# Kernel optimization log

Hardware: AMD Instinct MI355X
Metric: run time of the kernel (lower is better)

The kernel has to match this reference:

```python
import jax, jax.numpy as jnp
import numpy as np

TEMP = 0.07
EPS = 1e-8
THRESH = 0.0          # self.global_threshold default
NORM_EPS = 1e-12      # F.normalize default eps


def setup_inputs() -> dict:
    key = jax.random.key(0)
    k1, k2, k3 = jax.random.split(key, 3)
    T, C, H, W = 8, 256, 64, 64
    return {
        "current_preds": jax.random.uniform(k1, (T, 1, H, W), jnp.float32),
        "history_preds": jax.random.uniform(k2, (T, 1, H, W), jnp.float32),
        "features": jax.random.normal(k3, (T, C, H, W), jnp.float32),
        "epoch": 1,
    }


def _supervised_labels(current_preds, history_preds):
    # Deviation per video (Dice-like metrics on binarized preds), then select
    # current pred if dev <= threshold else history pred (both detached).
    T = current_preds.shape[0]
    cb = (current_preds > 0.5).astype(jnp.float32).reshape(T, -1)
    hb = (history_preds > 0.5).astype(jnp.float32).reshape(T, -1)
    e1 = (cb * hb).sum(axis=1)
    e2 = cb.sum(axis=1) + hb.sum(axis=1)
    m1 = (2.0 * e1 + EPS) / (e2 + EPS)
    m2 = (e1 + EPS) / (e2 - e1 + EPS)
    dev = 1.0 - (m1 + m2) / 2.0                       # [T]
    use_curr = (dev <= THRESH)[:, None, None, None]
    return jnp.where(use_curr, current_preds, history_preds)


def _contrastive_loss(features, labels):
    T, C, H, W = features.shape
    N = H * W
    feat = features.reshape(T, C, N).transpose(0, 2, 1)            # [T,N,C]
    nrm = jnp.linalg.norm(feat, axis=-1, keepdims=True)
    feat = feat / jnp.maximum(nrm, NORM_EPS)                       # L2 normalize
    lbl = labels.reshape(T, N)
    fg = lbl > 0.5
    bg = ~fg
    sim = jnp.einsum('tnc,tmc->tnm', feat, feat) / TEMP            # [T,N,N]
    pos = jnp.exp(jnp.diagonal(sim, axis1=1, axis2=2))             # [T,N]
    # neg_i = sum over bg columns of exp(sim); masked matvec honors fg/bg split
    neg = jnp.einsum('tnm,tm->tn', jnp.exp(sim), bg.astype(feat.dtype))
    per_pix = -jnp.log(pos / (pos + neg + EPS))                    # [T,N]
    fgf = fg.astype(feat.dtype)
    n_fg = fgf.sum(axis=1)
    frame_loss = (per_pix * fgf).sum(axis=1) / jnp.maximum(n_fg, 1.0)  # mean over fg
    valid = (fg.any(axis=1) & bg.any(axis=1)).astype(feat.dtype)   # frames with both
    n_valid = valid.sum()
    return jnp.where(n_valid > 0,
                     (frame_loss * valid).sum() / jnp.maximum(n_valid, 1.0),
                     jnp.zeros((), feat.dtype))


def reference(current_preds, history_preds, features, epoch):
    # epoch >= 1 path of DOC.forward (epoch==0 only populates memory)
    labels = jax.lax.stop_gradient(_supervised_labels(current_preds, history_preds))
    loss = _contrastive_loss(features, labels)
    return (labels, loss)
```

## Files before the change

kernel.cpp:

```cpp
#include <hip/hip_runtime.h>
#include <hip/hip_bf16.h>
#include <cstdint>
#include <cstddef>

constexpr int T = 8;
constexpr int C = 256;
constexpr int N = 4096;
constexpr int CAP = 4232;
constexpr float TEMP_INV = 14.285714285714286f;
constexpr float EPS = 1e-8f;

typedef __bf16 bf16;
typedef __bf16 bf16x8 __attribute__((ext_vector_type(8)));
typedef float floatx4 __attribute__((ext_vector_type(4)));

__device__ __forceinline__ void async_copy16(const bf16* g, bf16* l) {
    __builtin_amdgcn_global_load_lds((const __attribute__((address_space(1))) void*)g,
                                     (__attribute__((address_space(3))) void*)l,
                                     16, 0, 0);
}

__global__ void prep_kernel(const float* __restrict__ cur,
                            const float* __restrict__ hist,
                            float* __restrict__ out_labels,
                            float* __restrict__ negbuf,
                            unsigned short* __restrict__ rankmap,
                            bf16* __restrict__ fpack,
                            int* __restrict__ nfg, int* __restrict__ nbg) {
    int t = blockIdx.x;
    int tid = threadIdx.x;
    int lane = tid & 63;
    int w = tid >> 6;

    float cv[4], hv[4];
    float s1 = 0.f, sc = 0.f, sh = 0.f;
    #pragma unroll
    for (int it = 0; it < 4; ++it) {
        int p = it * 1024 + tid;
        float c = cur[t * N + p];
        float h = hist[t * N + p];
        cv[it] = c; hv[it] = h;
        float cb = c > 0.5f ? 1.f : 0.f;
        float hb = h > 0.5f ? 1.f : 0.f;
        s1 += cb * hb; sc += cb; sh += hb;
    }
    for (int o = 32; o > 0; o >>= 1) {
        s1 += __shfl_down(s1, o);
        sc += __shfl_down(sc, o);
        sh += __shfl_down(sh, o);
    }
    __shared__ float r1[16], r2[16], r3[16];
    __shared__ float uflag;
    __shared__ int cfg_s, cbg_s;
    if (lane == 0) { r1[w] = s1; r2[w] = sc; r3[w] = sh; }
    if (tid == 0) { cfg_s = 0; cbg_s = 0; }
    __syncthreads();
    if (tid == 0) {
        float e1 = 0.f, scs = 0.f, shs = 0.f;
        for (int i = 0; i < 16; ++i) { e1 += r1[i]; scs += r2[i]; shs += r3[i]; }
        float e2 = scs + shs;
        float m1 = (2.f * e1 + EPS) / (e2 + EPS);
        float m2 = (e1 + EPS) / (e2 - e1 + EPS);
        float dev = 1.f - 0.5f * (m1 + m2);
        uflag = (dev <= 0.0f) ? 1.f : 0.f;
    }
    __syncthreads();
    bool use_curr = uflag != 0.f;
    for (int it = 0; it < 4; ++it) {
        int p = it * 1024 + tid;
        int gi = t * N + p;
        float lab = use_curr ? cv[it] : hv[it];
        out_labels[gi] = lab;
        negbuf[gi] = 0.f;
        bool fg = lab > 0.5f;
        unsigned long long b = __ballot(fg);
        unsigned long long lowmask = (lane == 63) ? 0x7fffffffffffffffull
                                                  : ((1ull << lane) - 1ull);
        int rank_fg = __popcll(b & lowmask);
        int rank_bg = __popcll((~b) & lowmask);
        int cnt_fg = __popcll(b);
        int base_fg = 0, base_bg = 0;
        if (lane == 0) {
            base_fg = atomicAdd(&cfg_s, cnt_fg);
            base_bg = atomicAdd(&cbg_s, 64 - cnt_fg);
        }
        base_fg = __shfl(base_fg, 0);
        base_bg = __shfl(base_bg, 0);
        int rank = fg ? (base_fg + rank_fg) : (base_bg + rank_bg);
        rankmap[gi] = (unsigned short)(rank | (fg ? 0x8000 : 0));
    }
    __syncthreads();
    if (tid == 0) { nfg[t] = cfg_s; nbg[t] = cbg_s; }
    float4 z4 = make_float4(0.f, 0.f, 0.f, 0.f);
    float4* pz = (float4*)(fpack + ((size_t)t * CAP + N) * C);
    int chunks = (CAP - N) * (C / 8);
    for (int i = tid; i < chunks; i += 1024) pz[i] = z4;
}

__global__ __launch_bounds__(256, 4) void normalize_kernel(const float* __restrict__ feat,
                                                           const unsigned short* __restrict__ rankmap,
                                                           const int* __restrict__ nfg,
                                                           bf16* __restrict__ fpack,
                                                           float* __restrict__ posc) {
    __shared__ bf16 tile[64 * 258];
    __shared__ float partial[256];
    __shared__ float rnorm_s[64];
    __shared__ unsigned short rk_s[64];
    __shared__ int bbase_s;
    int t = blockIdx.x & 7;
    int n0 = (blockIdx.x >> 3) * 64;
    int tid = threadIdx.x;
    int lane63 = tid & 63;
    int w = tid >> 6;
    if (tid == 0) bbase_s = (nfg[t] + 7) & ~7;
    if (tid < 64) rk_s[tid] = rankmap[t * N + n0 + tid];
    const float* fb = feat + (size_t)t * C * N;
    float ss = 0.f;
    #pragma unroll 16
    for (int it = 0; it < 64; ++it) {
        int c = w * 64 + it;
        float v = fb[(size_t)c * N + n0 + lane63];
        ss += v * v;
        tile[lane63 * 258 + c] = (bf16)v;
    }
    partial[tid] = ss;
    __syncthreads();
    if (tid < 64) {
        float s = partial[tid] + partial[tid + 64] + partial[tid + 128] + partial[tid + 192];
        float r = 1.f / fmaxf(sqrtf(s), 1e-12f);
        rnorm_s[tid] = r;
        unsigned short rk = rk_s[tid];
        if (rk & 0x8000) posc[t * N + (rk & 0x7fff)] = s * r * r;
    }
    __syncthreads();
    int bbase = bbase_s;
    bf16* fp = fpack + (size_t)t * CAP * C;
    #pragma unroll
    for (int it = 0; it < 8; ++it) {
        int l = it * 256 + tid;
        int n = l >> 5;
        int c8 = l & 31;
        unsigned short rk = rk_s[n];
        int r_pack = (rk & 0x7fff) + ((rk & 0x8000) ? 0 : bbase);
        int slot = (c8 & ~7) | ((c8 & 7) ^ (r_pack & 7));
        float r = rnorm_s[n];
        bf16x8 vin = *(const bf16x8*)&tile[n * 258 + c8 * 8];
        bf16x8 vo;
        for (int j = 0; j < 8; ++j) vo[j] = (bf16)((float)vin[j] * r);
        *(bf16x8*)(fp + (size_t)r_pack * C + slot * 8) = vo;
    }
}

__global__ __launch_bounds__(256, 3) void sim_kernel(const bf16* __restrict__ fpack,
                                                     const int* __restrict__ nfg,
                                                     const int* __restrict__ nbg,
                                                     float* __restrict__ neg) {
    int t = blockIdx.x & 7;
    int wid = blockIdx.x >> 3;
    int nfgt = nfg[t];
    int nbgt = nbg[t];
    if (nfgt <= 0 || nbgt <= 0) return;
    int nr = (nfgt + 127) >> 7;
    int nc = (nbgt + 127) >> 7;
    if (wid >= nr * nc) return;
    int rowbase = (wid / nc) * 128;
    int colbase = (wid % nc) * 128;
    int bbase = (nfgt + 7) & ~7;

    __shared__ bf16 a_lds[128 * 64];
    __shared__ bf16 b_lds[128 * 64];
    int tid = threadIdx.x;
    int lane = tid & 63;
    int w = tid >> 6;
    const bf16* fb = fpack + (size_t)t * CAP * C;

    int lrow = lane >> 3;
    int lchunk = lane & 7;
    int r0w = (w & 1) * 64;
    int c0w = (w >> 1) * 64;

    floatx4 acc[4][4];
    for (int i = 0; i < 4; ++i)
        for (int j = 0; j < 4; ++j)
            acc[i][j] = (floatx4){0.f, 0.f, 0.f, 0.f};

    for (int ks = 0; ks < 4; ++ks) {
        int k0 = ks * 64;
        __syncthreads();
        for (int s = 0; s < 4; ++s) {
            int q = w * 4 + s;
            int ra = rowbase + q * 8 + lrow;
            int rb = bbase + colbase + q * 8 + lrow;
            async_copy16(fb + (size_t)ra * C + k0 + lchunk * 8, &a_lds[q * 512]);
            async_copy16(fb + (size_t)rb * C + k0 + lchunk * 8, &b_lds[q * 512]);
        }
        __syncthreads();
        for (int kk = 0; kk < 64; kk += 32) {
            int quad = lane >> 4;
            int chread = (kk >> 3) + quad;
            bf16x8 af[4], bfr[4];
            for (int i = 0; i < 4; ++i) {
                int r = r0w + 16 * i + (lane & 15);
                int chs = chread ^ (r & 7);
                af[i] = *(const bf16x8*)&a_lds[r * 64 + chs * 8];
            }
            for (int j = 0; j < 4; ++j) {
                int cidx = c0w + 16 * j + (lane & 15);
                int chs = chread ^ (cidx & 7);
                bfr[j] = *(const bf16x8*)&b_lds[cidx * 64 + chs * 8];
            }
            for (int i = 0; i < 4; ++i)
                for (int j = 0; j < 4; ++j)
                    acc[i][j] = __builtin_amdgcn_mfma_f32_16x16x32_bf16(af[i], bfr[j], acc[i][j], 0, 0, 0);
        }
    }

    float bgv[4];
    for (int j = 0; j < 4; ++j) {
        int cidx = colbase + c0w + 16 * j + (lane & 15);
        bgv[j] = (cidx < nbgt) ? 1.f : 0.f;
    }
    int quad = lane >> 4;
    for (int i = 0; i < 4; ++i) {
        for (int reg = 0; reg < 4; ++reg) {
            float msum = 0.f;
            for (int j = 0; j < 4; ++j)
                msum += __expf(acc[i][j][reg] * TEMP_INV) * bgv[j];
            msum += __shfl_xor(msum, 1);
            msum += __shfl_xor(msum, 2);
            msum += __shfl_xor(msum, 4);
            msum += __shfl_xor(msum, 8);
            if ((lane & 15) == 0) {
                int row = rowbase + r0w + 16 * i + quad * 4 + reg;
                if (row < nfgt) atomicAdd(&neg[t * N + row], msum);
            }
        }
    }
}

__global__ void loss_kernel(const float* __restrict__ negbuf,
                            const float* __restrict__ posc,
                            const int* __restrict__ nfg,
                            const int* __restrict__ nbg,
                            float* __restrict__ out_loss) {
    int tid = threadIdx.x;
    int t = tid >> 6;
    int lane = tid & 63;
    int nfgt = nfg[t];
    float s = 0.f;
    #pragma unroll 4
    for (int k = lane; k < nfgt; k += 64) {
        float pos = __expf(posc[t * N + k] * TEMP_INV);
        float ng = negbuf[t * N + k];
        s += logf((pos + ng + EPS) / pos);
    }
    for (int o = 32; o > 0; o >>= 1) s += __shfl_down(s, o);
    __shared__ float fl[8], vv[8];
    if (lane == 0) {
        float valid = (nfgt > 0 && nbg[t] > 0) ? 1.f : 0.f;
        fl[t] = valid * (s / fmaxf((float)nfgt, 1.f));
        vv[t] = valid;
    }
    __syncthreads();
    if (tid == 0) {
        float ls = 0.f, v = 0.f;
        for (int i = 0; i < T; ++i) { ls += fl[i]; v += vv[i]; }
        out_loss[0] = (v > 0.f) ? ls / fmaxf(v, 1.f) : 0.f;
    }
}

extern "C" void kernel_launch(void* const* d_in, const int* in_sizes, int n_in,
                              void* d_out, int out_size, void* d_ws, size_t ws_size,
                              hipStream_t stream) {
    const float* cur  = (const float*)d_in[0];
    const float* hist = (const float*)d_in[1];
    const float* feat = (const float*)d_in[2];
    float* out = (float*)d_out;

    char* ws = (char*)d_ws;
    bf16*  fpack   = (bf16*)ws;
    size_t off = (size_t)T * CAP * C * sizeof(bf16);
    float* negbuf  = (float*)(ws + off);  off += (size_t)T * N * 4;
    float* posc    = (float*)(ws + off);  off += (size_t)T * N * 4;
    unsigned short* rankmap = (unsigned short*)(ws + off); off += (size_t)T * N * 2;
    int*   nfg     = (int*)(ws + off);
    int*   nbg     = nfg + 8;

    prep_kernel<<<8, 1024, 0, stream>>>(cur, hist, out, negbuf, rankmap, fpack, nfg, nbg);
    normalize_kernel<<<512, 256, 0, stream>>>(feat, rankmap, nfg, fpack, posc);
    sim_kernel<<<2176, 256, 0, stream>>>(fpack, nfg, nbg, negbuf);
    loss_kernel<<<1, 512, 0, stream>>>(negbuf, posc, nfg, nbg, out + 32768);
}
```

Measured before the change: 150.0 us.

## Fuse label prep into pack kernel and fold loss into sim via last-block reduction

Each normalize block now recomputes the per-frame Dice statistics and its own prefix counts of foreground and background pixels. That lets it derive pack ranks locally, which removes the separate single-block prep kernel and the rankmap round trip. The loss reduction moves into the tail of sim_kernel, where the last finishing block (found with an atomic done counter) computes it, so the extra loss kernel launch goes away. In exchange every block redundantly scans the 4096 labels of its frame, and the final block does the reduction alone, serialized after the grid.

```diff
diff --git a/kernel.cpp b/kernel.cpp
--- a/kernel.cpp
+++ b/kernel.cpp
@@ -20,120 +20,101 @@
                                      16, 0, 0);
 }
 
-__global__ void prep_kernel(const float* __restrict__ cur,
-                            const float* __restrict__ hist,
-                            float* __restrict__ out_labels,
-                            float* __restrict__ negbuf,
-                            unsigned short* __restrict__ rankmap,
-                            bf16* __restrict__ fpack,
-                            int* __restrict__ nfg, int* __restrict__ nbg) {
-    int t = blockIdx.x;
+__global__ __launch_bounds__(256, 4) void pack_kernel(const float* __restrict__ cur,
+                                                      const float* __restrict__ hist,
+                                                      const float* __restrict__ feat,
+                                                      float* __restrict__ out_labels,
+                                                      float* __restrict__ negbuf,
+                                                      bf16* __restrict__ fpack,
+                                                      float* __restrict__ posc,
+                                                      int* __restrict__ nfg,
+                                                      int* __restrict__ nbg,
+                                                      int* __restrict__ done_ctr) {
+    __shared__ bf16 tile[64 * 258];
+    __shared__ float partial[256];
+    __shared__ float rbuf[4][5];
+    __shared__ float rnorm_s[64];
+    __shared__ unsigned short rk_s[64];
+    int t = blockIdx.x & 7;
+    int s = blockIdx.x >> 3;
+    int n0 = s * 64;
     int tid = threadIdx.x;
     int lane = tid & 63;
     int w = tid >> 6;
 
-    float cv[4], hv[4];
-    float s1 = 0.f, sc = 0.f, sh = 0.f;
-    #pragma unroll
-    for (int it = 0; it < 4; ++it) {
-        int p = it * 1024 + tid;
-        float c = cur[t * N + p];
-        float h = hist[t * N + p];
-        cv[it] = c; hv[it] = h;
+    const float* cb_ = cur + t * N;
+    const float* hb_ = hist + t * N;
+    float e1 = 0.f, sc = 0.f, sh = 0.f, pc = 0.f, ph = 0.f;
+    for (int p = tid; p < N; p += 256) {
+        float c = cb_[p], h = hb_[p];
         float cb = c > 0.5f ? 1.f : 0.f;
         float hb = h > 0.5f ? 1.f : 0.f;
-        s1 += cb * hb; sc += cb; sh += hb;
+        e1 += cb * hb; sc += cb; sh += hb;
+        if (p < n0) { pc += cb; ph += hb; }
     }
     for (int o = 32; o > 0; o >>= 1) {
-        s1 += __shfl_down(s1, o);
+        e1 += __shfl_down(e1, o);
         sc += __shfl_down(sc, o);
         sh += __shfl_down(sh, o);
-    }
-    __shared__ float r1[16], r2[16], r3[16];
-    __shared__ float uflag;
-    __shared__ int cfg_s, cbg_s;
-    if (lane == 0) { r1[w] = s1; r2[w] = sc; r3[w] = sh; }
-    if (tid == 0) { cfg_s = 0; cbg_s = 0; }
-    __syncthreads();
-    if (tid == 0) {
-        float e1 = 0.f, scs = 0.f, shs = 0.f;
-        for (int i = 0; i < 16; ++i) { e1 += r1[i]; scs += r2[i]; shs += r3[i]; }
-        float e2 = scs + shs;
-        float m1 = (2.f * e1 + EPS) / (e2 + EPS);
-        float m2 = (e1 + EPS) / (e2 - e1 + EPS);
-        float dev = 1.f - 0.5f * (m1 + m2);
-        uflag = (dev <= 0.0f) ? 1.f : 0.f;
-    }
-    __syncthreads();
-    bool use_curr = uflag != 0.f;
-    for (int it = 0; it < 4; ++it) {
-        int p = it * 1024 + tid;
-        int gi = t * N + p;
-        float lab = use_curr ? cv[it] : hv[it];
-        out_labels[gi] = lab;
-        negbuf[gi] = 0.f;
+        pc += __shfl_down(pc, o);
+        ph += __shfl_down(ph, o);
+    }
+    if (lane == 0) { rbuf[w][0]=e1; rbuf[w][1]=sc; rbuf[w][2]=sh; rbuf[w][3]=pc; rbuf[w][4]=ph; }
+    __syncthreads();
+    float E1 = rbuf[0][0]+rbuf[1][0]+rbuf[2][0]+rbuf[3][0];
+    float SC = rbuf[0][1]+rbuf[1][1]+rbuf[2][1]+rbuf[3][1];
+    float SH = rbuf[0][2]+rbuf[1][2]+rbuf[2][2]+rbuf[3][2];
+    float PC = rbuf[0][3]+rbuf[1][3]+rbuf[2][3]+rbuf[3][3];
+    float PH = rbuf[0][4]+rbuf[1][4]+rbuf[2][4]+rbuf[3][4];
+    float E2 = SC + SH;
+    float m1 = (2.f * E1 + EPS) / (E2 + EPS);
+    float m2 = (E1 + EPS) / (E2 - E1 + EPS);
+    float dev = 1.f - 0.5f * (m1 + m2);
+    bool uc = (dev <= 0.0f);
+    int nfgt  = (int)(uc ? SC : SH);
+    int nbgt  = N - nfgt;
+    int bbase = (nfgt + 7) & ~7;
+    int basef = (int)(uc ? PC : PH);
+    int baseb = n0 - basef;
+
+    if (blockIdx.x < 8 && tid == 0) { nfg[t] = nfgt; nbg[t] = nbgt; }
+    if (blockIdx.x == 0 && tid == 0) { *done_ctr = 0; }
+
+    if (tid < 64) {
+        int p = n0 + tid;
+        float lab = uc ? cb_[p] : hb_[p];
+        out_labels[t * N + p] = lab;
+        negbuf[t * N + p] = 0.f;
         bool fg = lab > 0.5f;
         unsigned long long b = __ballot(fg);
-        unsigned long long lowmask = (lane == 63) ? 0x7fffffffffffffffull
-                                                  : ((1ull << lane) - 1ull);
-        int rank_fg = __popcll(b & lowmask);
-        int rank_bg = __popcll((~b) & lowmask);
-        int cnt_fg = __popcll(b);
-        int base_fg = 0, base_bg = 0;
-        if (lane == 0) {
-            base_fg = atomicAdd(&cfg_s, cnt_fg);
-            base_bg = atomicAdd(&cbg_s, 64 - cnt_fg);
-        }
-        base_fg = __shfl(base_fg, 0);
-        base_bg = __shfl(base_bg, 0);
-        int rank = fg ? (base_fg + rank_fg) : (base_bg + rank_bg);
-        rankmap[gi] = (unsigned short)(rank | (fg ? 0x8000 : 0));
-    }
-    __syncthreads();
-    if (tid == 0) { nfg[t] = cfg_s; nbg[t] = cbg_s; }
-    float4 z4 = make_float4(0.f, 0.f, 0.f, 0.f);
-    float4* pz = (float4*)(fpack + ((size_t)t * CAP + N) * C);
-    int chunks = (CAP - N) * (C / 8);
-    for (int i = tid; i < chunks; i += 1024) pz[i] = z4;
-}
-
-__global__ __launch_bounds__(256, 4) void normalize_kernel(const float* __restrict__ feat,
-                                                           const unsigned short* __restrict__ rankmap,
-                                                           const int* __restrict__ nfg,
-                                                           bf16* __restrict__ fpack,
-                                                           float* __restrict__ posc) {
-    __shared__ bf16 tile[64 * 258];
-    __shared__ float partial[256];
-    __shared__ float rnorm_s[64];
-    __shared__ unsigned short rk_s[64];
-    __shared__ int bbase_s;
-    int t = blockIdx.x & 7;
-    int n0 = (blockIdx.x >> 3) * 64;
-    int tid = threadIdx.x;
-    int lane63 = tid & 63;
-    int w = tid >> 6;
-    if (tid == 0) bbase_s = (nfg[t] + 7) & ~7;
-    if (tid < 64) rk_s[tid] = rankmap[t * N + n0 + tid];
+        unsigned long long lowmask = (tid == 63) ? 0x7fffffffffffffffull
+                                                 : ((1ull << tid) - 1ull);
+        int rfg = __popcll(b & lowmask);
+        int rbg = __popcll((~b) & lowmask);
+        int rank = fg ? (basef + rfg) : (baseb + rbg);
+        rk_s[tid] = (unsigned short)(rank | (fg ? 0x8000 : 0));
+    }
+    __syncthreads();
+
     const float* fb = feat + (size_t)t * C * N;
     float ss = 0.f;
     #pragma unroll 16
     for (int it = 0; it < 64; ++it) {
         int c = w * 64 + it;
-        float v = fb[(size_t)c * N + n0 + lane63];
+        float v = fb[(size_t)c * N + n0 + lane];
         ss += v * v;
-        tile[lane63 * 258 + c] = (bf16)v;
+        tile[lane * 258 + c] = (bf16)v;
     }
     partial[tid] = ss;
     __syncthreads();
     if (tid < 64) {
-        float s = partial[tid] + partial[tid + 64] + partial[tid + 128] + partial[tid + 192];
-        float r = 1.f / fmaxf(sqrtf(s), 1e-12f);
+        float sv = partial[tid] + partial[tid + 64] + partial[tid + 128] + partial[tid + 192];
+        float r = 1.f / fmaxf(sqrtf(sv), 1e-12f);
         rnorm_s[tid] = r;
         unsigned short rk = rk_s[tid];
-        if (rk & 0x8000) posc[t * N + (rk & 0x7fff)] = s * r * r;
-    }
-    __syncthreads();
-    int bbase = bbase_s;
+        if (rk & 0x8000) posc[t * N + (rk & 0x7fff)] = sv * r * r;
+    }
+    __syncthreads();
     bf16* fp = fpack + (size_t)t * CAP * C;
     #pragma unroll
     for (int it = 0; it < 8; ++it) {
@@ -149,123 +130,139 @@
         for (int j = 0; j < 8; ++j) vo[j] = (bf16)((float)vin[j] * r);
         *(bf16x8*)(fp + (size_t)r_pack * C + slot * 8) = vo;
     }
+
+    int gstart = bbase + nbgt;
+    int nch = (CAP - gstart) * 32;
+    float4 z4 = make_float4(0.f, 0.f, 0.f, 0.f);
+    float4* pz = (float4*)(fpack + ((size_t)t * CAP + gstart) * C);
+    for (int i = s * 256 + tid; i < nch; i += 64 * 256) pz[i] = z4;
 }
 
 __global__ __launch_bounds__(256, 3) void sim_kernel(const bf16* __restrict__ fpack,
                                                      const int* __restrict__ nfg,
                                                      const int* __restrict__ nbg,
-                                                     float* __restrict__ neg) {
+                                                     float* __restrict__ neg,
+                                                     const float* __restrict__ posc,
+                                                     int* __restrict__ done_ctr,
+                                                     float* __restrict__ out_loss) {
     int t = blockIdx.x & 7;
     int wid = blockIdx.x >> 3;
-    int nfgt = nfg[t];
-    int nbgt = nbg[t];
-    if (nfgt <= 0 || nbgt <= 0) return;
-    int nr = (nfgt + 127) >> 7;
-    int nc = (nbgt + 127) >> 7;
-    if (wid >= nr * nc) return;
-    int rowbase = (wid / nc) * 128;
-    int colbase = (wid % nc) * 128;
-    int bbase = (nfgt + 7) & ~7;
-
-    __shared__ bf16 a_lds[128 * 64];
-    __shared__ bf16 b_lds[128 * 64];
     int tid = threadIdx.x;
     int lane = tid & 63;
     int w = tid >> 6;
-    const bf16* fb = fpack + (size_t)t * CAP * C;
-
-    int lrow = lane >> 3;
-    int lchunk = lane & 7;
-    int r0w = (w & 1) * 64;
-    int c0w = (w >> 1) * 64;
-
-    floatx4 acc[4][4];
-    for (int i = 0; i < 4; ++i)
-        for (int j = 0; j < 4; ++j)
-            acc[i][j] = (floatx4){0.f, 0.f, 0.f, 0.f};
-
-    for (int ks = 0; ks < 4; ++ks) {
-        int k0 = ks * 64;
-        __syncthreads();
-        for (int s = 0; s < 4; ++s) {
-            int q = w * 4 + s;
-            int ra = rowbase + q * 8 + lrow;
-            int rb = bbase + colbase + q * 8 + lrow;
-            async_copy16(fb + (size_t)ra * C + k0 + lchunk * 8, &a_lds[q * 512]);
-            async_copy16(fb + (size_t)rb * C + k0 + lchunk * 8, &b_lds[q * 512]);
+    int nfgt = nfg[t];
+    int nbgt = nbg[t];
+    bool active = (nfgt > 0 && nbgt > 0);
+    if (active) {
+        int nr = (nfgt + 127) >> 7;
+        int nc = (nbgt + 127) >> 7;
+        active = (wid < nr * nc);
+        if (active) {
+            int rowbase = (wid / nc) * 128;
+            int colbase = (wid % nc) * 128;
+            int bbase = (nfgt + 7) & ~7;
+
+            __shared__ bf16 a_lds[128 * 64];
+            __shared__ bf16 b_lds[128 * 64];
+            const bf16* fb = fpack + (size_t)t * CAP * C;
+
+            int lrow = lane >> 3;
+            int lchunk = lane & 7;
+            int r0w = (w & 1) * 64;
+            int c0w = (w >> 1) * 64;
+
+            floatx4 acc[4][4];
+            for (int i = 0; i < 4; ++i)
+                for (int j = 0; j < 4; ++j)
+                    acc[i][j] = (floatx4){0.f, 0.f, 0.f, 0.f};
+
+            for (int ks = 0; ks < 4; ++ks) {
+                int k0 = ks * 64;
+                __syncthreads();
+                for (int s = 0; s < 4; ++s) {
+                    int q = w * 4 + s;
+                    int ra = rowbase + q * 8 + lrow;
+                    int rb = bbase + colbase + q * 8 + lrow;
+                    async_copy16(fb + (size_t)ra * C + k0 + lchunk * 8, &a_lds[q * 512]);
+                    async_copy16(fb + (size_t)rb * C + k0 + lchunk * 8, &b_lds[q * 512]);
+                }
+                __syncthreads();
+                for (int kk = 0; kk < 64; kk += 32) {
+                    int quad = lane >> 4;
+                    int chread = (kk >> 3) + quad;
+                    bf16x8 af[4], bfr[4];
+                    for (int i = 0; i < 4; ++i) {
+                        int r = r0w + 16 * i + (lane & 15);
+                        int chs = chread ^ (r & 7);
+                        af[i] = *(const bf16x8*)&a_lds[r * 64 + chs * 8];
+                    }
+                    for (int j = 0; j < 4; ++j) {
+                        int cidx = c0w + 16 * j + (lane & 15);
+                        int chs = chread ^ (cidx & 7);
+                        bfr[j] = *(const bf16x8*)&b_lds[cidx * 64 + chs * 8];
+                    }
+                    for (int i = 0; i < 4; ++i)
+                        for (int j = 0; j < 4; ++j)
+                            acc[i][j] = __builtin_amdgcn_mfma_f32_16x16x32_bf16(af[i], bfr[j], acc[i][j], 0, 0, 0);
+                }
+            }
+
+            float bgv[4];
+            for (int j = 0; j < 4; ++j) {
+                int cidx = colbase + c0w + 16 * j + (lane & 15);
+                bgv[j] = (cidx < nbgt) ? 1.f : 0.f;
+            }
+            int quad = lane >> 4;
+            for (int i = 0; i < 4; ++i) {
+                for (int reg = 0; reg < 4; ++reg) {
+                    float msum = 0.f;
+                    for (int j = 0; j < 4; ++j)
+                        msum += __expf(acc[i][j][reg] * TEMP_INV) * bgv[j];
+                    msum += __shfl_xor(msum, 1);
+                    msum += __shfl_xor(msum, 2);
+                    msum += __shfl_xor(msum, 4);
+                    msum += __shfl_xor(msum, 8);
+                    if ((lane & 15) == 0) {
+                        int row = rowbase + r0w + 16 * i + quad * 4 + reg;
+                        if (row < nfgt) atomicAdd(&neg[t * N + row], msum);
+                    }
+                }
+            }
+        }
+    }
+
+    __threadfence();
+    __shared__ int lastflag;
+    if (tid == 0) {
+        int old = atomicAdd(done_ctr, 1);
+        lastflag = (old == (int)gridDim.x - 1) ? 1 : 0;
+    }
+    __syncthreads();
+    if (lastflag) {
+        __threadfence();
+        __shared__ float fl[8], vv[8];
+        for (int tf = w; tf < 8; tf += 4) {
+            int nf = nfg[tf];
+            float s = 0.f;
+            #pragma unroll 4
+            for (int k = lane; k < nf; k += 64) {
+                float pos = __expf(posc[tf * N + k] * TEMP_INV);
+                float ng = neg[tf * N + k];
+                s += logf((pos + ng + EPS) / pos);
+            }
+            for (int o = 32; o > 0; o >>= 1) s += __shfl_down(s, o);
+            if (lane == 0) {
+                float valid = (nf > 0 && nbg[tf] > 0) ? 1.f : 0.f;
+                fl[tf] = valid * (s / fmaxf((float)nf, 1.f));
+                vv[tf] = valid;
+            }
         }
         __syncthreads();
-        for (int kk = 0; kk < 64; kk += 32) {
-            int quad = lane >> 4;
-            int chread = (kk >> 3) + quad;
-            bf16x8 af[4], bfr[4];
-            for (int i = 0; i < 4; ++i) {
-                int r = r0w + 16 * i + (lane & 15);
-                int chs = chread ^ (r & 7);
-                af[i] = *(const bf16x8*)&a_lds[r * 64 + chs * 8];
-            }
-            for (int j = 0; j < 4; ++j) {
-                int cidx = c0w + 16 * j + (lane & 15);
-                int chs = chread ^ (cidx & 7);
-                bfr[j] = *(const bf16x8*)&b_lds[cidx * 64 + chs * 8];
-            }
-            for (int i = 0; i < 4; ++i)
-                for (int j = 0; j < 4; ++j)
-                    acc[i][j] = __builtin_amdgcn_mfma_f32_16x16x32_bf16(af[i], bfr[j], acc[i][j], 0, 0, 0);
+        if (tid == 0) {
+            float ls = 0.f, v = 0.f;
+            for (int i = 0; i < T; ++i) { ls += fl[i]; v += vv[i]; }
+            out_loss[0] = (v > 0.f) ? ls / fmaxf(v, 1.f) : 0.f;
         }
-    }
-
-    float bgv[4];
-    for (int j = 0; j < 4; ++j) {
-        int cidx = colbase + c0w + 16 * j + (lane & 15);
-        bgv[j] = (cidx < nbgt) ? 1.f : 0.f;
-    }
-    int quad = lane >> 4;
-    for (int i = 0; i < 4; ++i) {
-        for (int reg = 0; reg < 4; ++reg) {
-            float msum = 0.f;
-            for (int j = 0; j < 4; ++j)
-                msum += __expf(acc[i][j][reg] * TEMP_INV) * bgv[j];
-            msum += __shfl_xor(msum, 1);
-            msum += __shfl_xor(msum, 2);
-            msum += __shfl_xor(msum, 4);
-            msum += __shfl_xor(msum, 8);
-            if ((lane & 15) == 0) {
-                int row = rowbase + r0w + 16 * i + quad * 4 + reg;
-                if (row < nfgt) atomicAdd(&neg[t * N + row], msum);
-            }
-        }
-    }
-}
-
-__global__ void loss_kernel(const float* __restrict__ negbuf,
-                            const float* __restrict__ posc,
-                            const int* __restrict__ nfg,
-                            const int* __restrict__ nbg,
-                            float* __restrict__ out_loss) {
-    int tid = threadIdx.x;
-    int t = tid >> 6;
-    int lane = tid & 63;
-    int nfgt = nfg[t];
-    float s = 0.f;
-    #pragma unroll 4
-    for (int k = lane; k < nfgt; k += 64) {
-        float pos = __expf(posc[t * N + k] * TEMP_INV);
-        float ng = negbuf[t * N + k];
-        s += logf((pos + ng + EPS) / pos);
-    }
-    for (int o = 32; o > 0; o >>= 1) s += __shfl_down(s, o);
-    __shared__ float fl[8], vv[8];
-    if (lane == 0) {
-        float valid = (nfgt > 0 && nbg[t] > 0) ? 1.f : 0.f;
-        fl[t] = valid * (s / fmaxf((float)nfgt, 1.f));
-        vv[t] = valid;
-    }
-    __syncthreads();
-    if (tid == 0) {
-        float ls = 0.f, v = 0.f;
-        for (int i = 0; i < T; ++i) { ls += fl[i]; v += vv[i]; }
-        out_loss[0] = (v > 0.f) ? ls / fmaxf(v, 1.f) : 0.f;
     }
 }
 
@@ -282,12 +279,12 @@
     size_t off = (size_t)T * CAP * C * sizeof(bf16);
     float* negbuf  = (float*)(ws + off);  off += (size_t)T * N * 4;
     float* posc    = (float*)(ws + off);  off += (size_t)T * N * 4;
-    unsigned short* rankmap = (unsigned short*)(ws + off); off += (size_t)T * N * 2;
-    int*   nfg     = (int*)(ws + off);
-    int*   nbg     = nfg + 8;
-
-    prep_kernel<<<8, 1024, 0, stream>>>(cur, hist, out, negbuf, rankmap, fpack, nfg, nbg);
-    normalize_kernel<<<512, 256, 0, stream>>>(feat, rankmap, nfg, fpack, posc);
-    sim_kernel<<<2176, 256, 0, stream>>>(fpack, nfg, nbg, negbuf);
-    loss_kernel<<<1, 512, 0, stream>>>(negbuf, posc, nfg, nbg, out + 32768);
-}
+    int*   nfg     = (int*)(ws + off);    off += 8 * 4;
+    int*   nbg     = (int*)(ws + off);    off += 8 * 4;
+    int*   done_ctr = (int*)(ws + off);
+
+    pack_kernel<<<512, 256, 0, stream>>>(cur, hist, feat, out, negbuf, fpack,
+                                         posc, nfg, nbg, done_ctr);
+    sim_kernel<<<2176, 256, 0, stream>>>(fpack, nfg, nbg, negbuf, posc,
+                                         done_ctr, out + 32768);
+}
```

Result: slower. 260.3 us (+73.5%).
